# Kernel tuning notes

Hardware: AMD Instinct MI355X
Metric: run time of the kernel (lower is better)

Reference implementation:

```python
import jax, jax.numpy as jnp
import numpy as np

B, H, W, C, NUM_HEADS = 32, 8, 128, 512, 8
HK, WK = 7, 11  # local_k
N = H * W
HEAD_DIM = C // NUM_HEADS
SCALE = HEAD_DIM ** (-0.5)


def make_local_mask():
    # key (i,j) is visible to query (h,w) iff i+HK//2 in [h, h+HK) and j+WK//2 in [w, w+WK)
    dh = jnp.arange(H)[None, :] - jnp.arange(H)[:, None] + HK // 2  # [H(query), H(key)]
    dw = jnp.arange(W)[None, :] - jnp.arange(W)[:, None] + WK // 2  # [W(query), W(key)]
    ok_h = (dh >= 0) & (dh < HK)
    ok_w = (dw >= 0) & (dw < WK)
    ok = ok_h[:, None, :, None] & ok_w[None, :, None, :]  # [H,W,H,W]
    return jnp.where(ok.reshape(N, N), 0.0, -jnp.inf).astype(jnp.float32)


def setup_inputs() -> dict:
    key = jax.random.key(0)
    k1, k2, k3 = jax.random.split(key, 3)
    s = C ** (-0.5)
    return {
        "x": jax.random.normal(k1, (B, N, C), dtype=jnp.float32),
        "w_qkv": jax.random.normal(k2, (C, 3 * C), dtype=jnp.float32) * s,
        "w_proj": jax.random.normal(k3, (C, C), dtype=jnp.float32) * s,
        "b_proj": jnp.zeros((C,), dtype=jnp.float32),
    }


def reference(x, w_qkv, w_proj, b_proj):
    mask = make_local_mask()  # [N, N], 0 in window, -inf outside
    b, n, c = x.shape
    qkv = (x @ w_qkv).reshape(b, n, 3, NUM_HEADS, HEAD_DIM)
    qkv = jnp.transpose(qkv, (2, 0, 3, 1, 4))  # [3, B, heads, N, head_dim]
    q, k, v = qkv[0], qkv[1], qkv[2]
    attn = jnp.einsum('bhqd,bhkd->bhqk', q, k) * SCALE + mask
    attn = jax.nn.softmax(attn, axis=-1)
    out = jnp.einsum('bhqk,bhkd->bhqd', attn, v)
    out = jnp.transpose(out, (0, 2, 1, 3)).reshape(b, n, c)
    return out @ w_proj + b_proj
```

## Files before the change

kernel.cpp:

```cpp
#include <hip/hip_runtime.h>

#define Bsz   32
#define Hh    8
#define Ww    128
#define Cc    512
#define NHEAD 8
#define HD    64
#define NN    1024
#define SCALE 0.125f
#define ROWS  1536

typedef _Float16 f16x8 __attribute__((ext_vector_type(8)));
typedef float    f32x4 __attribute__((ext_vector_type(4)));

__device__ __forceinline__ void gload16(const _Float16* g, _Float16* l) {
#if __has_builtin(__builtin_amdgcn_global_load_lds)
  __builtin_amdgcn_global_load_lds(
      (const __attribute__((address_space(1))) unsigned int*)g,
      (__attribute__((address_space(3))) unsigned int*)l, 16, 0, 0);
#else
  *(uint4*)l = *(const uint4*)g;
#endif
}

__global__ __launch_bounds__(256) void tcvt(
    const float* __restrict__ in, _Float16* __restrict__ out, int Nn, int K) {
  const int id = blockIdx.x * 256 + threadIdx.x;
  if (id < Nn * K) {
    const int n = id / K, k = id - n * K;
    out[id] = (_Float16)in[(size_t)k * Nn + n];
  }
}

template<bool A_F32, bool OUT_F16, bool HAS_BIAS>
__global__ __launch_bounds__(256, 2) void gemm_mfma(
    const void* __restrict__ Ap,
    const _Float16* __restrict__ BT,
    const float* __restrict__ bias,
    void* __restrict__ Cout,
    int nbx, int Nn, int K)
{
  __shared__ _Float16 As[128 * 32];
  __shared__ _Float16 Bs[128 * 32];

  const int wg    = blockIdx.x;
  const int chunk = gridDim.x >> 3;
  const int nid   = (wg & 7) * chunk + (wg >> 3);
  const int bn    = (nid % nbx) * 128;
  const int bm    = (nid / nbx) * 128;

  const int t  = threadIdx.x;
  const int l  = t & 63, wv = t >> 6;
  const int wr = wv >> 1, wc = wv & 1;

  f32x4 acc[4][4] = {};

  const int arow = t >> 2;
  const int ac   = (t & 3) * 8;

  for (int k0 = 0; k0 < K; k0 += 32) {
    __syncthreads();
    if constexpr (A_F32) {
      const float* Af = (const float*)Ap;
#pragma unroll
      for (int rr = 0; rr < 2; ++rr) {
        const float* src = &Af[(size_t)(bm + arow + rr * 64) * K + k0 + ac];
        const float4 f0 = *(const float4*)src;
        const float4 f1 = *(const float4*)(src + 4);
        union { _Float16 h[8]; uint4 u; } pk;
        pk.h[0] = (_Float16)f0.x; pk.h[1] = (_Float16)f0.y;
        pk.h[2] = (_Float16)f0.z; pk.h[3] = (_Float16)f0.w;
        pk.h[4] = (_Float16)f1.x; pk.h[5] = (_Float16)f1.y;
        pk.h[6] = (_Float16)f1.z; pk.h[7] = (_Float16)f1.w;
        *(uint4*)&As[(arow + rr * 64) * 32 + ac] = pk.u;
      }
    } else {
      const _Float16* Ah = (const _Float16*)Ap;
      gload16(Ah + (size_t)(bm + arow)      * K + k0 + ac, &As[t * 8]);
      gload16(Ah + (size_t)(bm + 64 + arow) * K + k0 + ac, &As[2048 + t * 8]);
    }
    gload16(BT + (size_t)(bn + arow)      * K + k0 + ac, &Bs[t * 8]);
    gload16(BT + (size_t)(bn + 64 + arow) * K + k0 + ac, &Bs[2048 + t * 8]);
    __syncthreads();

    const int rA = l & 15, ks = (l >> 4) * 8;
    f16x8 aF[4], bF[4];
#pragma unroll
    for (int i = 0; i < 4; ++i)
      aF[i] = *(const f16x8*)&As[(wr * 64 + i * 16 + rA) * 32 + ks];
#pragma unroll
    for (int j = 0; j < 4; ++j)
      bF[j] = *(const f16x8*)&Bs[(wc * 64 + j * 16 + rA) * 32 + ks];
#pragma unroll
    for (int i = 0; i < 4; ++i)
#pragma unroll
      for (int j = 0; j < 4; ++j)
        acc[i][j] = __builtin_amdgcn_mfma_f32_16x16x32_f16(aF[i], bF[j], acc[i][j], 0, 0, 0);
  }

  const int lc = l & 15, lr4 = (l >> 4) * 4;
#pragma unroll
  for (int i = 0; i < 4; ++i) {
    const size_t row0 = (size_t)(bm + wr * 64 + i * 16 + lr4);
#pragma unroll
    for (int j = 0; j < 4; ++j) {
      const int col = bn + wc * 64 + j * 16 + lc;
      const float bv = HAS_BIAS ? bias[col] : 0.f;
#pragma unroll
      for (int r = 0; r < 4; ++r) {
        const float v = acc[i][j][r] + bv;
        if (OUT_F16)
          ((_Float16*)Cout)[(row0 + r) * Nn + col] = (_Float16)v;
        else
          ((float*)Cout)[(row0 + r) * Nn + col] = v;
      }
    }
  }
}

__global__ __launch_bounds__(512, 4) void local_attn_mfma(
    const _Float16* __restrict__ qkv, _Float16* __restrict__ outh)
{
  const int wg  = blockIdx.x + (Hh / 2) * (blockIdx.y + NHEAD * blockIdx.z);
  const int nid = ((wg & 7) << 7) + (wg >> 3);
  const int hp = nid & 3, head = (nid >> 2) & 7, b = nid >> 5;
  const int h0 = hp * 2;

  const int t = threadIdx.x;
  const int wv = t >> 6, l = t & 63;
  const int g = l >> 4, c = l & 15;
  const int w0 = wv * 16;
  const int kb = min(max(w0 - 8, 0), 96);

  __shared__ _Float16 Vsh[64 * 132];
  __shared__ _Float16 Pbuf[8][576];

  const _Float16* qb = qkv + (size_t)b * NN * ROWS;

  f16x8 qF[2][2];
#pragma unroll
  for (int hi = 0; hi < 2; ++hi) {
    const _Float16* Qg = qb + (size_t)((h0 + hi) * Ww + w0 + c) * ROWS + head * HD;
    qF[hi][0] = *(const f16x8*)&Qg[g * 8];
    qF[hi][1] = *(const f16x8*)&Qg[32 + g * 8];
  }

  float mbias[2][4];
#pragma unroll
  for (int tt = 0; tt < 2; ++tt)
#pragma unroll
    for (int r = 0; r < 4; ++r) {
      const int kcol = kb + 16 * tt + 4 * g + r;
      const int qq   = w0 + c;
      mbias[tt][r] = (kcol >= qq - 5 && kcol <= qq + 5) ? 0.f : -1e30f;
    }

  const int r0 = max(0, h0 - 3), r1 = min(Hh - 1, h0 + 4);
  float m_run[2] = {-1e30f, -1e30f}, s_run[2] = {0.f, 0.f};
  f32x4 accO[2][4] = {};

  const int dd = t & 7, cg = (t & 255) >> 3;

  for (int kr = r0; kr <= r1; ++kr) {
    __syncthreads();
    if (t < 256) {
      f16x8 vr[4];
      const _Float16* Vg = qb + (size_t)(kr * Ww + cg * 4) * ROWS + 2 * Cc + head * HD + dd * 8;
#pragma unroll
      for (int i = 0; i < 4; ++i)
        vr[i] = *(const f16x8*)&Vg[(size_t)i * ROWS];
#pragma unroll
      for (int e = 0; e < 8; ++e) {
        union { _Float16 hh[4]; uint2 u; } pk;
        pk.hh[0] = vr[0][e]; pk.hh[1] = vr[1][e];
        pk.hh[2] = vr[2][e]; pk.hh[3] = vr[3][e];
        *(uint2*)&Vsh[(dd * 8 + e) * 132 + cg * 4] = pk.u;
      }
    }
    __syncthreads();

    const _Float16* Kg = qb + (size_t)(kr * Ww) * ROWS + Cc + head * HD;

#pragma unroll
    for (int hi = 0; hi < 2; ++hi) {
      const int hq = h0 + hi;
      if (kr < hq - 3 || kr > hq + 3) continue;

      f32x4 accS[2] = {};
#pragma unroll
      for (int tt = 0; tt < 2; ++tt) {
        const int col = kb + 16 * tt + c;
#pragma unroll
        for (int s = 0; s < 2; ++s) {
          const f16x8 kF = *(const f16x8*)&Kg[(size_t)col * ROWS + (s * 4 + g) * 8];
          accS[tt] = __builtin_amdgcn_mfma_f32_16x16x32_f16(kF, qF[hi][s], accS[tt], 0, 0, 0);
        }
      }

      float sc[2][4];
      float smax = -1e30f;
#pragma unroll
      for (int tt = 0; tt < 2; ++tt)
#pragma unroll
        for (int r = 0; r < 4; ++r) {
          sc[tt][r] = __builtin_fmaf(accS[tt][r], SCALE, mbias[tt][r]);
          smax = fmaxf(smax, sc[tt][r]);
        }
      smax = fmaxf(smax, __shfl_xor(smax, 16));
      smax = fmaxf(smax, __shfl_xor(smax, 32));
      const float mnew  = fmaxf(m_run[hi], smax);
      const float alpha = __expf(m_run[hi] - mnew);
      m_run[hi] = mnew;

      float ps = 0.f;
#pragma unroll
      for (int tt = 0; tt < 2; ++tt) {
        float p0 = __expf(sc[tt][0] - mnew), p1 = __expf(sc[tt][1] - mnew);
        float p2 = __expf(sc[tt][2] - mnew), p3 = __expf(sc[tt][3] - mnew);
        ps += (p0 + p1) + (p2 + p3);
        union { _Float16 hh[4]; uint2 u; } pk;
        pk.hh[0] = (_Float16)p0; pk.hh[1] = (_Float16)p1;
        pk.hh[2] = (_Float16)p2; pk.hh[3] = (_Float16)p3;
        *(uint2*)&Pbuf[wv][c * 36 + 16 * tt + 4 * g] = pk.u;
      }
      ps += __shfl_xor(ps, 16);
      ps += __shfl_xor(ps, 32);
      s_run[hi] = s_run[hi] * alpha + ps;

      float alr[4];
#pragma unroll
      for (int r = 0; r < 4; ++r)
        alr[r] = __shfl(alpha, 4 * g + r, 16);

      asm volatile("s_waitcnt lgkmcnt(0)" ::: "memory");

      union { f16x8 v; uint2 u2[2]; } pF;
      {
        const _Float16* pp = &Pbuf[wv][c * 36 + g * 8];
        pF.u2[0] = *(const uint2*)pp;
        pF.u2[1] = *(const uint2*)(pp + 4);
      }
#pragma unroll
      for (int jj = 0; jj < 4; ++jj)
#pragma unroll
        for (int r = 0; r < 4; ++r) accO[hi][jj][r] *= alr[r];
#pragma unroll
      for (int jj = 0; jj < 4; ++jj) {
        union { f16x8 v; uint2 u2[2]; } vF;
        const _Float16* vp = &Vsh[(16 * jj + c) * 132 + kb + g * 8];
        vF.u2[0] = *(const uint2*)vp;
        vF.u2[1] = *(const uint2*)(vp + 4);
        accO[hi][jj] = __builtin_amdgcn_mfma_f32_16x16x32_f16(pF.v, vF.v, accO[hi][jj], 0, 0, 0);
      }
    }
  }

#pragma unroll
  for (int hi = 0; hi < 2; ++hi) {
    _Float16* ob = outh + ((size_t)b * NN + (h0 + hi) * Ww + w0) * Cc + head * HD;
#pragma unroll
    for (int r = 0; r < 4; ++r) {
      const float sr  = __shfl(s_run[hi], 4 * g + r, 16);
      const float inv = 1.f / sr;
      const int q = 4 * g + r;
#pragma unroll
      for (int jj = 0; jj < 4; ++jj)
        ob[(size_t)q * Cc + 16 * jj + c] = (_Float16)(accO[hi][jj][r] * inv);
    }
  }
}

extern "C" void kernel_launch(void* const* d_in, const int* in_sizes, int n_in,
                              void* d_out, int out_size, void* d_ws, size_t ws_size,
                              hipStream_t stream)
{
  const float* x      = (const float*)d_in[0];
  const float* w_qkv  = (const float*)d_in[1];
  const float* w_proj = (const float*)d_in[2];
  const float* b_proj = (const float*)d_in[3];
  float* out = (float*)d_out;

  const int M = Bsz * NN;
  char* ws = (char*)d_ws;
  _Float16* qkvh  = (_Float16*)ws;
  _Float16* attnh = (_Float16*)(ws + 100663296);
  _Float16* wqT   = (_Float16*)(ws + 134217728);
  _Float16* wpT   = (_Float16*)(ws + 134217728 + 1572864);

  tcvt<<<(ROWS * Cc + 255) / 256, 256, 0, stream>>>(w_qkv, wqT, ROWS, Cc);
  tcvt<<<(Cc * Cc + 255) / 256, 256, 0, stream>>>(w_proj, wpT, Cc, Cc);

  gemm_mfma<true, true, false><<<(ROWS / 128) * (M / 128), 256, 0, stream>>>(
      x, wqT, nullptr, qkvh, ROWS / 128, ROWS, Cc);

  local_attn_mfma<<<dim3(Hh / 2, NHEAD, Bsz), 512, 0, stream>>>(qkvh, attnh);

  gemm_mfma<false, false, true><<<(Cc / 128) * (M / 128), 256, 0, stream>>>(
      attnh, wpT, b_proj, out, Cc / 128, Cc, Cc);
}
```

Before: 194.4 us.

## Double-buffer GEMM shared-memory tiles to overlap global loads with MFMA

Adds a second LDS buffer for the A and B tiles of the MFMA GEMM. The loads for the next K-slice are issued before the current slice's MFMAs. For the fp32 A path, the values are held in registers and converted and written after compute. This cuts one barrier per iteration and hides global-load latency behind the matrix math, at the cost of twice the LDS footprint and extra registers, which may lower occupancy at the two-block launch bound.

New measurement: 194.4 us. No clear change (-0.0%).

```diff
diff --git a/kernel.cpp b/kernel.cpp
--- a/kernel.cpp
+++ b/kernel.cpp
@@ -40,8 +40,8 @@
     void* __restrict__ Cout,
     int nbx, int Nn, int K)
 {
-  __shared__ _Float16 As[128 * 32];
-  __shared__ _Float16 Bs[128 * 32];
+  __shared__ _Float16 As[2][128 * 32];
+  __shared__ _Float16 Bs[2][128 * 32];
 
   const int wg    = blockIdx.x;
   const int chunk = gridDim.x >> 3;
@@ -58,44 +58,75 @@
   const int arow = t >> 2;
   const int ac   = (t & 3) * 8;
 
-  for (int k0 = 0; k0 < K; k0 += 32) {
-    __syncthreads();
-    if constexpr (A_F32) {
-      const float* Af = (const float*)Ap;
-#pragma unroll
-      for (int rr = 0; rr < 2; ++rr) {
-        const float* src = &Af[(size_t)(bm + arow + rr * 64) * K + k0 + ac];
-        const float4 f0 = *(const float4*)src;
-        const float4 f1 = *(const float4*)(src + 4);
-        union { _Float16 h[8]; uint4 u; } pk;
-        pk.h[0] = (_Float16)f0.x; pk.h[1] = (_Float16)f0.y;
-        pk.h[2] = (_Float16)f0.z; pk.h[3] = (_Float16)f0.w;
-        pk.h[4] = (_Float16)f1.x; pk.h[5] = (_Float16)f1.y;
-        pk.h[6] = (_Float16)f1.z; pk.h[7] = (_Float16)f1.w;
-        *(uint4*)&As[(arow + rr * 64) * 32 + ac] = pk.u;
-      }
-    } else {
-      const _Float16* Ah = (const _Float16*)Ap;
-      gload16(Ah + (size_t)(bm + arow)      * K + k0 + ac, &As[t * 8]);
-      gload16(Ah + (size_t)(bm + 64 + arow) * K + k0 + ac, &As[2048 + t * 8]);
-    }
-    gload16(BT + (size_t)(bn + arow)      * K + k0 + ac, &Bs[t * 8]);
-    gload16(BT + (size_t)(bn + 64 + arow) * K + k0 + ac, &Bs[2048 + t * 8]);
-    __syncthreads();
+  float4 a0, a1, a2, a3;
+
+  const float*    Af = (const float*)Ap;
+  const _Float16* Ah = (const _Float16*)Ap;
+
+  auto issueA = [&](int k0) {
+    const float* s0 = &Af[(size_t)(bm + arow)      * K + k0 + ac];
+    const float* s1 = &Af[(size_t)(bm + arow + 64) * K + k0 + ac];
+    a0 = *(const float4*)s0; a1 = *(const float4*)(s0 + 4);
+    a2 = *(const float4*)s1; a3 = *(const float4*)(s1 + 4);
+  };
+  auto writeA = [&](int pb) {
+    union { _Float16 h[8]; uint4 u; } p0, p1;
+    p0.h[0] = (_Float16)a0.x; p0.h[1] = (_Float16)a0.y;
+    p0.h[2] = (_Float16)a0.z; p0.h[3] = (_Float16)a0.w;
+    p0.h[4] = (_Float16)a1.x; p0.h[5] = (_Float16)a1.y;
+    p0.h[6] = (_Float16)a1.z; p0.h[7] = (_Float16)a1.w;
+    p1.h[0] = (_Float16)a2.x; p1.h[1] = (_Float16)a2.y;
+    p1.h[2] = (_Float16)a2.z; p1.h[3] = (_Float16)a2.w;
+    p1.h[4] = (_Float16)a3.x; p1.h[5] = (_Float16)a3.y;
+    p1.h[6] = (_Float16)a3.z; p1.h[7] = (_Float16)a3.w;
+    *(uint4*)&As[pb][arow * 32 + ac]        = p0.u;
+    *(uint4*)&As[pb][(arow + 64) * 32 + ac] = p1.u;
+  };
+  auto gloadA = [&](int k0, int pb) {
+    gload16(Ah + (size_t)(bm + arow)      * K + k0 + ac, &As[pb][t * 8]);
+    gload16(Ah + (size_t)(bm + 64 + arow) * K + k0 + ac, &As[pb][2048 + t * 8]);
+  };
+  auto gloadB = [&](int k0, int pb) {
+    gload16(BT + (size_t)(bn + arow)      * K + k0 + ac, &Bs[pb][t * 8]);
+    gload16(BT + (size_t)(bn + 64 + arow) * K + k0 + ac, &Bs[pb][2048 + t * 8]);
+  };
+
+  const int nt = K / 32;
+
+  if constexpr (A_F32) { issueA(0); writeA(0); }
+  else                 { gloadA(0, 0); }
+  gloadB(0, 0);
+  __syncthreads();
+
+  int buf = 0;
+  for (int tt = 0; tt < nt; ++tt) {
+    const int k0n = (tt + 1) * 32;
+    const bool more = (tt + 1 < nt);
+    if (more) {
+      if constexpr (A_F32) issueA(k0n);
+      else                 gloadA(k0n, buf ^ 1);
+      gloadB(k0n, buf ^ 1);
+    }
 
     const int rA = l & 15, ks = (l >> 4) * 8;
     f16x8 aF[4], bF[4];
 #pragma unroll
     for (int i = 0; i < 4; ++i)
-      aF[i] = *(const f16x8*)&As[(wr * 64 + i * 16 + rA) * 32 + ks];
+      aF[i] = *(const f16x8*)&As[buf][(wr * 64 + i * 16 + rA) * 32 + ks];
 #pragma unroll
     for (int j = 0; j < 4; ++j)
-      bF[j] = *(const f16x8*)&Bs[(wc * 64 + j * 16 + rA) * 32 + ks];
+      bF[j] = *(const f16x8*)&Bs[buf][(wc * 64 + j * 16 + rA) * 32 + ks];
 #pragma unroll
     for (int i = 0; i < 4; ++i)
 #pragma unroll
       for (int j = 0; j < 4; ++j)
         acc[i][j] = __builtin_amdgcn_mfma_f32_16x16x32_f16(aF[i], bF[j], acc[i][j], 0, 0, 0);
+
+    if (more) {
+      if constexpr (A_F32) writeA(buf ^ 1);
+    }
+    __syncthreads();
+    buf ^= 1;
   }
 
   const int lc = l & 15, lr4 = (l >> 4) * 4;
```

## Double-buffer GEMM tiles, widen to 128x256 with 8 waves, pre-convert x to fp16

Applied to the files above, without the earlier changes.

The GEMM kernel now uses 512 threads with a 128x256 output tile and double-buffered LDS, issuing the next K-slice's async global-to-LDS loads before the MFMAs on the current slice, and synchronising once per iteration. The fp32-to-fp16 conversion of x moves out of the GEMM into a separate vectorized kernel, so both GEMMs take fp16 A through direct LDS loads. The aim is to hide load latency and raise reuse of the B tile. The cost is an extra pass over x in memory, plus higher LDS and register use per block, which may reduce occupancy.

Result: no change. 196.0 us (+0.8%).

```diff
diff --git a/kernel.cpp b/kernel.cpp
--- a/kernel.cpp
+++ b/kernel.cpp
@@ -23,6 +23,21 @@
 #endif
 }
 
+__global__ __launch_bounds__(256) void cvt_f32_f16(
+    const float* __restrict__ in, _Float16* __restrict__ out, int n8) {
+  const int i = blockIdx.x * 256 + threadIdx.x;
+  if (i < n8) {
+    const float4 f0 = ((const float4*)in)[(size_t)i * 2];
+    const float4 f1 = ((const float4*)in)[(size_t)i * 2 + 1];
+    union { _Float16 h[8]; uint4 u; } pk;
+    pk.h[0] = (_Float16)f0.x; pk.h[1] = (_Float16)f0.y;
+    pk.h[2] = (_Float16)f0.z; pk.h[3] = (_Float16)f0.w;
+    pk.h[4] = (_Float16)f1.x; pk.h[5] = (_Float16)f1.y;
+    pk.h[6] = (_Float16)f1.z; pk.h[7] = (_Float16)f1.w;
+    ((uint4*)out)[i] = pk.u;
+  }
+}
+
 __global__ __launch_bounds__(256) void tcvt(
     const float* __restrict__ in, _Float16* __restrict__ out, int Nn, int K) {
   const int id = blockIdx.x * 256 + threadIdx.x;
@@ -32,70 +47,63 @@
   }
 }
 
-template<bool A_F32, bool OUT_F16, bool HAS_BIAS>
-__global__ __launch_bounds__(256, 2) void gemm_mfma(
-    const void* __restrict__ Ap,
+template<bool OUT_F16, bool HAS_BIAS>
+__global__ __launch_bounds__(512, 4) void gemm_mfma(
+    const _Float16* __restrict__ A,
     const _Float16* __restrict__ BT,
     const float* __restrict__ bias,
     void* __restrict__ Cout,
     int nbx, int Nn, int K)
 {
-  __shared__ _Float16 As[128 * 32];
-  __shared__ _Float16 Bs[128 * 32];
+  __shared__ _Float16 As[2][128 * 32];
+  __shared__ _Float16 Bs[2][256 * 32];
 
   const int wg    = blockIdx.x;
   const int chunk = gridDim.x >> 3;
   const int nid   = (wg & 7) * chunk + (wg >> 3);
-  const int bn    = (nid % nbx) * 128;
+  const int bn    = (nid % nbx) * 256;
   const int bm    = (nid / nbx) * 128;
 
   const int t  = threadIdx.x;
   const int l  = t & 63, wv = t >> 6;
-  const int wr = wv >> 1, wc = wv & 1;
+  const int wr = wv >> 2, wc = wv & 3;
 
   f32x4 acc[4][4] = {};
 
   const int arow = t >> 2;
   const int ac   = (t & 3) * 8;
 
-  for (int k0 = 0; k0 < K; k0 += 32) {
-    __syncthreads();
-    if constexpr (A_F32) {
-      const float* Af = (const float*)Ap;
-#pragma unroll
-      for (int rr = 0; rr < 2; ++rr) {
-        const float* src = &Af[(size_t)(bm + arow + rr * 64) * K + k0 + ac];
-        const float4 f0 = *(const float4*)src;
-        const float4 f1 = *(const float4*)(src + 4);
-        union { _Float16 h[8]; uint4 u; } pk;
-        pk.h[0] = (_Float16)f0.x; pk.h[1] = (_Float16)f0.y;
-        pk.h[2] = (_Float16)f0.z; pk.h[3] = (_Float16)f0.w;
-        pk.h[4] = (_Float16)f1.x; pk.h[5] = (_Float16)f1.y;
-        pk.h[6] = (_Float16)f1.z; pk.h[7] = (_Float16)f1.w;
-        *(uint4*)&As[(arow + rr * 64) * 32 + ac] = pk.u;
-      }
-    } else {
-      const _Float16* Ah = (const _Float16*)Ap;
-      gload16(Ah + (size_t)(bm + arow)      * K + k0 + ac, &As[t * 8]);
-      gload16(Ah + (size_t)(bm + 64 + arow) * K + k0 + ac, &As[2048 + t * 8]);
-    }
-    gload16(BT + (size_t)(bn + arow)      * K + k0 + ac, &Bs[t * 8]);
-    gload16(BT + (size_t)(bn + 64 + arow) * K + k0 + ac, &Bs[2048 + t * 8]);
-    __syncthreads();
+  auto stage = [&](int k0, int pb) {
+    gload16(A  + (size_t)(bm + arow)       * K + k0 + ac, &As[pb][arow * 32 + ac]);
+    gload16(BT + (size_t)(bn + arow)       * K + k0 + ac, &Bs[pb][arow * 32 + ac]);
+    gload16(BT + (size_t)(bn + 128 + arow) * K + k0 + ac, &Bs[pb][(128 + arow) * 32 + ac]);
+  };
+
+  const int nt = K / 32;
+
+  stage(0, 0);
+  __syncthreads();
+
+  int buf = 0;
+  for (int tt = 0; tt < nt; ++tt) {
+    if (tt + 1 < nt) stage((tt + 1) * 32, buf ^ 1);
 
     const int rA = l & 15, ks = (l >> 4) * 8;
     f16x8 aF[4], bF[4];
 #pragma unroll
     for (int i = 0; i < 4; ++i)
-      aF[i] = *(const f16x8*)&As[(wr * 64 + i * 16 + rA) * 32 + ks];
+      aF[i] = *(const f16x8*)&As[buf][(wr * 64 + i * 16 + rA) * 32 + ks];
 #pragma unroll
     for (int j = 0; j < 4; ++j)
-      bF[j] = *(const f16x8*)&Bs[(wc * 64 + j * 16 + rA) * 32 + ks];
+      bF[j] = *(const f16x8*)&Bs[buf][(wc * 64 + j * 16 + rA) * 32 + ks];
 #pragma unroll
     for (int i = 0; i < 4; ++i)
 #pragma unroll
       for (int j = 0; j < 4; ++j)
         acc[i][j] = __builtin_amdgcn_mfma_f32_16x16x32_f16(aF[i], bF[j], acc[i][j], 0, 0, 0);
+
+    __syncthreads();
+    buf ^= 1;
   }
 
   const int lc = l & 15, lr4 = (l >> 4) * 4;
@@ -282,19 +290,21 @@
 
   const int M = Bsz * NN;
   char* ws = (char*)d_ws;
-  _Float16* qkvh  = (_Float16*)ws;
-  _Float16* attnh = (_Float16*)(ws + 100663296);
-  _Float16* wqT   = (_Float16*)(ws + 134217728);
-  _Float16* wpT   = (_Float16*)(ws + 134217728 + 1572864);
-
+  _Float16* xh    = (_Float16*)ws;
+  _Float16* qkvh  = (_Float16*)(ws + 33554432);
+  _Float16* attnh = (_Float16*)(ws + 134217728);
+  _Float16* wqT   = (_Float16*)(ws + 167772160);
+  _Float16* wpT   = (_Float16*)(ws + 167772160 + 1572864);
+
+  cvt_f32_f16<<<(M * Cc / 8 + 255) / 256, 256, 0, stream>>>(x, xh, M * Cc / 8);
   tcvt<<<(ROWS * Cc + 255) / 256, 256, 0, stream>>>(w_qkv, wqT, ROWS, Cc);
   tcvt<<<(Cc * Cc + 255) / 256, 256, 0, stream>>>(w_proj, wpT, Cc, Cc);
 
-  gemm_mfma<true, true, false><<<(ROWS / 128) * (M / 128), 256, 0, stream>>>(
-      x, wqT, nullptr, qkvh, ROWS / 128, ROWS, Cc);
+  gemm_mfma<true, false><<<(ROWS / 256) * (M / 128), 512, 0, stream>>>(
+      xh, wqT, nullptr, qkvh, ROWS / 256, ROWS, Cc);
 
   local_attn_mfma<<<dim3(Hh / 2, NHEAD, Bsz), 512, 0, stream>>>(qkvh, attnh);
 
-  gemm_mfma<false, false, true><<<(Cc / 128) * (M / 128), 256, 0, stream>>>(
-      attnh, wpT, b_proj, out, Cc / 128, Cc, Cc);
-}
+  gemm_mfma<false, true><<<(Cc / 256) * (M / 128), 512, 0, stream>>>(
+      attnh, wpT, b_proj, out, Cc / 256, Cc, Cc);
+}
```
